# Kernel optimization log

Measured on AMD Instinct MI355X. Metric: run time of the kernel, lower is better.

The kernel has to match this reference:

```python
import jax, jax.numpy as jnp
import numpy as np

jax.config.update("jax_enable_x64", True)

B, H, W = 16384, 19, 19
MAX_FLOOD = min(H * W // 4, 100)  # = 90, as in the torch module


def _count_neighbors(m):
    # m: [B,H,W] float. Sum of 4 orthogonal neighbors (zero-padded edges).
    up = jnp.pad(m[:, :-1, :], ((0, 0), (1, 0), (0, 0)))
    down = jnp.pad(m[:, 1:, :], ((0, 0), (0, 1), (0, 0)))
    left = jnp.pad(m[:, :, :-1], ((0, 0), (0, 0), (1, 0)))
    right = jnp.pad(m[:, :, 1:], ((0, 0), (0, 0), (0, 1)))
    return up + down + left + right


def _dilate(m):
    # m: [B,H,W] bool. OR of 4 orthogonal neighbors (False-padded edges).
    up = jnp.pad(m[:, :-1, :], ((0, 0), (1, 0), (0, 0)))
    down = jnp.pad(m[:, 1:, :], ((0, 0), (0, 1), (0, 0)))
    left = jnp.pad(m[:, :, :-1], ((0, 0), (0, 0), (1, 0)))
    right = jnp.pad(m[:, :, 1:], ((0, 0), (0, 0), (0, 1)))
    return up | down | left | right


def _flood_fill(seeds, mask):
    # Iterative neighbor expansion within mask, bounded iters + early exit.
    def cond(st):
        _, changed, i = st
        return changed & (i < MAX_FLOOD)

    def body(st):
        g, _, i = st
        exp = _dilate(g) & mask & ~g
        return (g | exp, exp.any(), i + 1)

    g, _, _ = jax.lax.while_loop(cond, body, (seeds, seeds.any(), jnp.int32(0)))
    return g


def setup_inputs() -> dict:
    key = jax.random.key(0)
    k1, k2, k3, k4, k5, k6 = jax.random.split(key, 6)
    # 0 = empty, 1 = black, 2 = white (planes never overlap)
    board = jax.random.randint(k1, (B, H, W), 0, 3)
    stones = jnp.stack([board == 1, board == 2], axis=1).astype(jnp.float32)
    current_player = jax.random.randint(k2, (B,), 0, 2).astype(jnp.int32)
    ko_rc = jax.random.randint(k3, (B, 2), 0, H).astype(jnp.int32)
    has_ko = jax.random.uniform(k4, (B,)) < 0.25
    ko_points = jnp.where(has_ko[:, None], ko_rc, jnp.int32(-1))
    hmax = np.iinfo(np.int64).max
    zobrist_stones = jax.random.randint(k5, (2, H, W), 0, hmax, dtype=jnp.int64)
    zobrist_turn = jax.random.randint(k6, (2,), 0, hmax, dtype=jnp.int64)
    position_hash = jnp.zeros((B,), jnp.int64)
    return {
        "stones": stones,
        "current_player": current_player,
        "ko_points": ko_points,
        "zobrist_stones": zobrist_stones,
        "zobrist_turn": zobrist_turn,
        "position_hash": position_hash,
    }


def reference(stones, current_player, ko_points, zobrist_stones, zobrist_turn, position_hash):
    stones_b = stones > 0.5                       # [B,2,H,W] bool
    empty_f = 1.0 - stones.sum(axis=1)            # [B,H,W] float (0/1)
    empty = ~stones_b.any(axis=1)                 # empty_mask
    liberties = _count_neighbors(empty_f)         # float liberty count per point

    # legal = empty points with at least one empty neighbor
    legal = empty & (liberties > 0.0)

    # capture moves: opponent stones with exactly one liberty
    cp = current_player.astype(jnp.int32)
    opp = jnp.take_along_axis(stones_b, (1 - cp)[:, None, None, None], axis=1)[:, 0]
    vulnerable = opp & (jnp.round(liberties).astype(jnp.int32) == 1)
    cap = empty & (_count_neighbors(vulnerable.astype(jnp.float32)) > 0.0)
    legal = legal | cap

    # ko restriction: mask the single ko point per game (if set)
    valid_ko = ko_points[:, 0] >= 0
    r_eq = jnp.arange(H)[None, :, None] == ko_points[:, 0][:, None, None]
    c_eq = jnp.arange(W)[None, None, :] == ko_points[:, 1][:, None, None]
    legal = legal & ~(valid_ko[:, None, None] & r_eq & c_eq)

    # flood fill the full groups-in-atari within opponent stones
    groups = _flood_fill(vulnerable, opp)

    # zobrist hash: XOR of stone hashes over the board + turn toggle
    contrib = jnp.where(stones_b, zobrist_stones[None], jnp.int64(0))  # [B,2,H,W]
    board_hash = jax.lax.reduce(contrib, np.int64(0), jax.lax.bitwise_xor, (1, 2, 3))
    new_hash = position_hash ^ board_hash ^ zobrist_turn[cp] ^ zobrist_turn[1 - cp]

    return (liberties, legal, groups, new_hash)
```

## Files before the change

kernel.cpp:

```cpp
#include <hip/hip_runtime.h>
#include <stdint.h>

#define WW 19
#define NP 361
#define M19 0x7FFFFu
#define BPB 16
#define TPB 256
#define BBSTR 25
#define PLSTR 97

__device__ __forceinline__ uint32_t rev19(uint32_t x) { return __brev(x) >> 13; }

__device__ __forceinline__ uint32_t runfill(uint32_t g, uint32_t m) {
  const uint32_t up = g | (m & ((m + g) ^ m ^ g));
  const uint32_t rm = rev19(m);
  const uint32_t rg = rev19(g);
  const uint32_t dn = rg | (rm & ((rm + rg) ^ rm ^ rg));
  return up | rev19(dn);
}

__global__ __launch_bounds__(TPB, 2) void go_fused(
    const float* __restrict__ stones, const int* __restrict__ cur,
    const int* __restrict__ ko, const int* __restrict__ zob,
    const int* __restrict__ zturn, const int* __restrict__ phash,
    float* __restrict__ out, int B) {
  __shared__ uint32_t bbuf[BPB * BBSTR];
  __shared__ uint32_t pl[BPB * PLSTR];

  const int wid = threadIdx.x >> 6;
  const int lane = threadIdx.x & 63;
  const int b0 = blockIdx.x * BPB;
  const size_t NB = (size_t)B * NP;

  int zb[6], zw[6];
#pragma unroll
  for (int i = 0; i < 6; ++i) {
    const int p = i * 64 + lane;
    zb[i] = (p < NP) ? zob[p] : 0;
    zw[i] = (p < NP) ? zob[NP + p] : 0;
  }
  const int zt = zturn[0] ^ zturn[1];

  int acc[4];
#pragma unroll
  for (int k = 0; k < 4; ++k) {
    const int lb = wid * 4 + k;
    const int b = b0 + lb;
    acc[k] = 0;
    if (b < B) {
      const float* sb = stones + (size_t)b * (2 * NP);
#pragma unroll
      for (int i = 0; i < 6; ++i) {
        const int p = i * 64 + lane;
        const bool inb = p < NP;
        const float bv = inb ? sb[p] : 0.0f;
        const float wv = inb ? sb[NP + p] : 0.0f;
        const bool bs = bv > 0.5f, wsn = wv > 0.5f;
        const uint64_t bbm = __ballot(bs);
        const uint64_t wbm = __ballot(wsn);
        if (lane < 4) {
          const uint64_t src = (lane < 2) ? bbm : wbm;
          const uint32_t vv = (lane & 1) ? (uint32_t)(src >> 32) : (uint32_t)src;
          bbuf[lb * BBSTR + i * 4 + lane] = vv;
        }
        acc[k] ^= zb[i] & (bs ? -1 : 0);
        acc[k] ^= zw[i] & (wsn ? -1 : 0);
      }
    }
  }
#pragma unroll
  for (int off = 32; off > 0; off >>= 1) {
#pragma unroll
    for (int k = 0; k < 4; ++k) acc[k] ^= __shfl_xor(acc[k], off, 64);
  }
  if (lane == 0) {
#pragma unroll
    for (int k = 0; k < 4; ++k) {
      const int b = b0 + wid * 4 + k;
      if (b < B) out[3 * NB + b] = (float)(phash[b] ^ acc[k] ^ zt);
    }
  }
  __syncthreads();

  if (threadIdx.x < BPB) {
    const int lb = threadIdx.x;
    const int b = b0 + lb;
    if (b < B) {
      uint64_t bmw[6], wmw[6];
#pragma unroll
      for (int i = 0; i < 6; ++i) {
        const uint32_t* q = &bbuf[lb * BBSTR + 4 * i];
        bmw[i] = (uint64_t)q[0] | ((uint64_t)q[1] << 32);
        wmw[i] = (uint64_t)q[2] | ((uint64_t)q[3] << 32);
      }
      const int cp = cur[b];
      uint32_t m[WW], e[WW];
#pragma unroll
      for (int r = 0; r < WW; ++r) {
        const int bit = WW * r;
        const int w = bit >> 6, sh = bit & 63;
        uint64_t xb = bmw[w] >> sh;
        uint64_t xw = wmw[w] >> sh;
        if (sh > 45) { xb |= bmw[w + 1] << (64 - sh); xw |= wmw[w + 1] << (64 - sh); }
        const uint32_t br = (uint32_t)xb & M19;
        const uint32_t wr = (uint32_t)xw & M19;
        m[r] = (cp == 0) ? wr : br;
        e[r] = ~(br | wr) & M19;
      }

      uint32_t* pb = &pl[lb * PLSTR];
      uint32_t vul[WW];
#pragma unroll
      for (int r = 0; r < WW; ++r) {
        const uint32_t u = (r > 0) ? e[r - 1] : 0u;
        const uint32_t d = (r < WW - 1) ? e[r + 1] : 0u;
        const uint32_t l = (e[r] << 1) & M19;
        const uint32_t rr = e[r] >> 1;
        const uint32_t s1 = u ^ d, c1 = u & d;
        const uint32_t s2 = l ^ rr, c2 = l & rr;
        const uint32_t cc = s1 & s2;
        const uint32_t L0 = s1 ^ s2;
        const uint32_t L1 = c1 ^ c2 ^ cc;
        pb[r] = L0;
        pb[19 + r] = L1;
        pb[38 + r] = (c1 & c2) | (cc & (c1 | c2));
        vul[r] = m[r] & L0 & ~L1;
      }

      const int2 kk = ((const int2*)ko)[b];
#pragma unroll
      for (int r = 0; r < WW; ++r) {
        const uint32_t u = (r > 0) ? e[r - 1] : 0u;
        const uint32_t d = (r < WW - 1) ? e[r + 1] : 0u;
        const uint32_t nbv = ((r > 0) ? vul[r - 1] : 0u) |
                             ((r < WW - 1) ? vul[r + 1] : 0u) |
                             ((vul[r] << 1) & M19) | (vul[r] >> 1);
        uint32_t leg = e[r] & (u | d | ((e[r] << 1) & M19) | (e[r] >> 1));
        leg |= e[r] & nbv;
        if (kk.x == r) leg &= ~(1u << kk.y);
        pb[57 + r] = leg;
      }

      uint32_t g[WW];
#pragma unroll
      for (int r = 0; r < WW; ++r) g[r] = runfill(vul[r], m[r]);
      for (int it = 0; it < 45; ++it) {
        uint32_t chg = 0, prev = 0;
#pragma unroll
        for (int r = 0; r < WW; ++r) {
          uint32_t t = g[r] | (prev & m[r]);
          t = runfill(t, m[r]);
          chg |= t ^ g[r];
          g[r] = t;
          prev = t;
        }
        prev = 0;
#pragma unroll
        for (int r = WW - 1; r >= 0; --r) {
          uint32_t t = g[r] | (prev & m[r]);
          t = runfill(t, m[r]);
          chg |= t ^ g[r];
          g[r] = t;
          prev = t;
        }
        if (!__any(chg != 0u)) break;
      }
#pragma unroll
      for (int r = 0; r < WW; ++r) pb[76 + r] = g[r];
    }
  }
  __syncthreads();

  if (b0 + BPB <= B) {
    float4* s0 = (float4*)(out + (size_t)b0 * NP);
    float4* s1 = (float4*)(out + NB + (size_t)b0 * NP);
    float4* s2 = (float4*)(out + 2 * NB + (size_t)b0 * NP);
    const int nq = BPB * NP / 4;
    for (int q = threadIdx.x; q < nq; q += TPB) {
      float t0[4], t1[4], t2[4];
#pragma unroll
      for (int j = 0; j < 4; ++j) {
        const int id = q * 4 + j;
        const int lb = (id * 92949) >> 25;
        const int p = id - lb * NP;
        const int r = (p * 27) >> 9;
        const int c = p - r * WW;
        const uint32_t* pb = &pl[lb * PLSTR];
        const uint32_t l0 = (pb[r] >> c) & 1u;
        const uint32_t l1 = (pb[19 + r] >> c) & 1u;
        const uint32_t l2 = (pb[38 + r] >> c) & 1u;
        t0[j] = (float)(l0 + 2u * l1 + 4u * l2);
        t1[j] = (float)((pb[57 + r] >> c) & 1u);
        t2[j] = (float)((pb[76 + r] >> c) & 1u);
      }
      s0[q] = make_float4(t0[0], t0[1], t0[2], t0[3]);
      s1[q] = make_float4(t1[0], t1[1], t1[2], t1[3]);
      s2[q] = make_float4(t2[0], t2[1], t2[2], t2[3]);
    }
  } else {
#pragma unroll
    for (int k = 0; k < 4; ++k) {
      const int lb = wid * 4 + k;
      const int b = b0 + lb;
      if (b < B) {
        float* o0 = out + (size_t)b * NP;
        const uint32_t* pb = &pl[lb * PLSTR];
#pragma unroll
        for (int i = 0; i < 6; ++i) {
          const int p = i * 64 + lane;
          if (p < NP) {
            const int r = (p * 27) >> 9;
            const int c = p - r * WW;
            const uint32_t l0 = (pb[r] >> c) & 1u;
            const uint32_t l1 = (pb[19 + r] >> c) & 1u;
            const uint32_t l2 = (pb[38 + r] >> c) & 1u;
            o0[p] = (float)(l0 + 2u * l1 + 4u * l2);
            o0[NB + p] = (float)((pb[57 + r] >> c) & 1u);
            o0[2 * NB + p] = (float)((pb[76 + r] >> c) & 1u);
          }
        }
      }
    }
  }
}

extern "C" void kernel_launch(void* const* d_in, const int* in_sizes, int n_in,
                              void* d_out, int out_size, void* d_ws,
                              size_t ws_size, hipStream_t stream) {
  const float* stones = (const float*)d_in[0];
  const int* cur = (const int*)d_in[1];
  const int* ko = (const int*)d_in[2];
  const int* zob = (const int*)d_in[3];
  const int* zturn = (const int*)d_in[4];
  const int* phash = (const int*)d_in[5];
  float* out = (float*)d_out;

  const int B = in_sizes[0] / (2 * NP);
  const int blocks = (B + BPB - 1) / BPB;
  go_fused<<<blocks, TPB, 0, stream>>>(stones, cur, ko, zob, zturn, phash, out,
                                       B);
}
```

Measured before the change: 32.74 us.

## Parallelize per-board bitboard work across lanes, one lane per row

Previously only 16 threads per block ran the liberty, legality and flood-fill work, one thread per board looping over all 19 rows. Now each wave handles 3 boards with one lane per row (57 active lanes), exchanging neighbor rows through wave shuffles. The flood fill becomes a parallel row-step iteration with a wave-wide exit check, and occupancy bounds rise to 4. The trade-off is that the fill may need more iterations than the old up/down sweep, blocks shrink to 12 boards, and 7 lanes per wave sit idle.

Result: faster. 29.76 us (-9.1%).

```diff
diff --git a/kernel.cpp b/kernel.cpp
--- a/kernel.cpp
+++ b/kernel.cpp
@@ -4,7 +4,9 @@
 #define WW 19
 #define NP 361
 #define M19 0x7FFFFu
-#define BPB 16
+#define BPW 3
+#define NWAVES 4
+#define BPB (BPW * NWAVES)
 #define TPB 256
 #define BBSTR 25
 #define PLSTR 97
@@ -19,7 +21,7 @@
   return up | rev19(dn);
 }
 
-__global__ __launch_bounds__(TPB, 2) void go_fused(
+__global__ __launch_bounds__(TPB, 4) void go_fused(
     const float* __restrict__ stones, const int* __restrict__ cur,
     const int* __restrict__ ko, const int* __restrict__ zob,
     const int* __restrict__ zturn, const int* __restrict__ phash,
@@ -41,10 +43,10 @@
   }
   const int zt = zturn[0] ^ zturn[1];
 
-  int acc[4];
-#pragma unroll
-  for (int k = 0; k < 4; ++k) {
-    const int lb = wid * 4 + k;
+  int acc[BPW];
+#pragma unroll
+  for (int k = 0; k < BPW; ++k) {
+    const int lb = wid * BPW + k;
     const int b = b0 + lb;
     acc[k] = 0;
     if (b < B) {
@@ -71,102 +73,90 @@
 #pragma unroll
   for (int off = 32; off > 0; off >>= 1) {
 #pragma unroll
-    for (int k = 0; k < 4; ++k) acc[k] ^= __shfl_xor(acc[k], off, 64);
+    for (int k = 0; k < BPW; ++k) acc[k] ^= __shfl_xor(acc[k], off, 64);
   }
   if (lane == 0) {
 #pragma unroll
-    for (int k = 0; k < 4; ++k) {
-      const int b = b0 + wid * 4 + k;
+    for (int k = 0; k < BPW; ++k) {
+      const int b = b0 + wid * BPW + k;
       if (b < B) out[3 * NB + b] = (float)(phash[b] ^ acc[k] ^ zt);
     }
   }
   __syncthreads();
 
-  if (threadIdx.x < BPB) {
-    const int lb = threadIdx.x;
+  {
+    const int k = (lane * 27) >> 9;
+    const int r = lane - k * WW;
+    const int lb = wid * BPW + k;
     const int b = b0 + lb;
-    if (b < B) {
-      uint64_t bmw[6], wmw[6];
-#pragma unroll
-      for (int i = 0; i < 6; ++i) {
-        const uint32_t* q = &bbuf[lb * BBSTR + 4 * i];
-        bmw[i] = (uint64_t)q[0] | ((uint64_t)q[1] << 32);
-        wmw[i] = (uint64_t)q[2] | ((uint64_t)q[3] << 32);
-      }
-      const int cp = cur[b];
-      uint32_t m[WW], e[WW];
-#pragma unroll
-      for (int r = 0; r < WW; ++r) {
-        const int bit = WW * r;
-        const int w = bit >> 6, sh = bit & 63;
-        uint64_t xb = bmw[w] >> sh;
-        uint64_t xw = wmw[w] >> sh;
-        if (sh > 45) { xb |= bmw[w + 1] << (64 - sh); xw |= wmw[w + 1] << (64 - sh); }
-        const uint32_t br = (uint32_t)xb & M19;
-        const uint32_t wr = (uint32_t)xw & M19;
-        m[r] = (cp == 0) ? wr : br;
-        e[r] = ~(br | wr) & M19;
-      }
-
+    const bool vl = (lane < 57) && (b < B);
+    const int lbs = vl ? lb : 0;
+    const int bsafe = vl ? b : (B - 1);
+
+    const int cp = cur[bsafe];
+    const int2 kk = ((const int2*)ko)[bsafe];
+
+    uint32_t mrow, erow;
+    {
+      const int bit = WW * r;
+      const int w = bit >> 6, sh = bit & 63;
+      const uint32_t* q = &bbuf[lbs * BBSTR + 4 * w];
+      const uint64_t Blo = (uint64_t)q[0] | ((uint64_t)q[1] << 32);
+      const uint64_t Wlo = (uint64_t)q[2] | ((uint64_t)q[3] << 32);
+      uint32_t br = (uint32_t)(Blo >> sh);
+      uint32_t wr = (uint32_t)(Wlo >> sh);
+      if (sh > 45) {
+        const uint64_t Bhi = (uint64_t)q[4] | ((uint64_t)q[5] << 32);
+        const uint64_t Whi = (uint64_t)q[6] | ((uint64_t)q[7] << 32);
+        br |= (uint32_t)(Bhi << (64 - sh));
+        wr |= (uint32_t)(Whi << (64 - sh));
+      }
+      br &= M19;
+      wr &= M19;
+      mrow = vl ? ((cp == 0) ? wr : br) : 0u;
+      erow = vl ? (~(br | wr) & M19) : 0u;
+    }
+
+    uint32_t t;
+    t = __shfl(erow, lane - 1, 64);
+    const uint32_t eu = (r > 0) ? t : 0u;
+    t = __shfl(erow, lane + 1, 64);
+    const uint32_t ed = (r < 18) ? t : 0u;
+    const uint32_t el = (erow << 1) & M19;
+    const uint32_t er_ = erow >> 1;
+    const uint32_t s1 = eu ^ ed, c1 = eu & ed;
+    const uint32_t s2 = el ^ er_, c2 = el & er_;
+    const uint32_t cc = s1 & s2;
+    const uint32_t L0 = s1 ^ s2;
+    const uint32_t L1 = c1 ^ c2 ^ cc;
+    const uint32_t L2 = (c1 & c2) | (cc & (c1 | c2));
+    uint32_t leg = erow & (eu | ed | el | er_);
+    const uint32_t vul = mrow & L0 & ~L1;
+    t = __shfl(vul, lane - 1, 64);
+    const uint32_t vu = (r > 0) ? t : 0u;
+    t = __shfl(vul, lane + 1, 64);
+    const uint32_t vd = (r < 18) ? t : 0u;
+    leg |= erow & (vu | vd | ((vul << 1) & M19) | (vul >> 1));
+    if (kk.x == r) leg &= ~(1u << kk.y);
+
+    uint32_t g = runfill(vul, mrow);
+    for (int it = 0; it < 90; ++it) {
+      t = __shfl(g, lane - 1, 64);
+      const uint32_t gu = (r > 0) ? t : 0u;
+      t = __shfl(g, lane + 1, 64);
+      const uint32_t gd = (r < 18) ? t : 0u;
+      const uint32_t gn = runfill(g | ((gu | gd) & mrow), mrow);
+      if (!__any(gn != g)) break;
+      g = gn;
+    }
+
+    if (vl) {
       uint32_t* pb = &pl[lb * PLSTR];
-      uint32_t vul[WW];
-#pragma unroll
-      for (int r = 0; r < WW; ++r) {
-        const uint32_t u = (r > 0) ? e[r - 1] : 0u;
-        const uint32_t d = (r < WW - 1) ? e[r + 1] : 0u;
-        const uint32_t l = (e[r] << 1) & M19;
-        const uint32_t rr = e[r] >> 1;
-        const uint32_t s1 = u ^ d, c1 = u & d;
-        const uint32_t s2 = l ^ rr, c2 = l & rr;
-        const uint32_t cc = s1 & s2;
-        const uint32_t L0 = s1 ^ s2;
-        const uint32_t L1 = c1 ^ c2 ^ cc;
-        pb[r] = L0;
-        pb[19 + r] = L1;
-        pb[38 + r] = (c1 & c2) | (cc & (c1 | c2));
-        vul[r] = m[r] & L0 & ~L1;
-      }
-
-      const int2 kk = ((const int2*)ko)[b];
-#pragma unroll
-      for (int r = 0; r < WW; ++r) {
-        const uint32_t u = (r > 0) ? e[r - 1] : 0u;
-        const uint32_t d = (r < WW - 1) ? e[r + 1] : 0u;
-        const uint32_t nbv = ((r > 0) ? vul[r - 1] : 0u) |
-                             ((r < WW - 1) ? vul[r + 1] : 0u) |
-                             ((vul[r] << 1) & M19) | (vul[r] >> 1);
-        uint32_t leg = e[r] & (u | d | ((e[r] << 1) & M19) | (e[r] >> 1));
-        leg |= e[r] & nbv;
-        if (kk.x == r) leg &= ~(1u << kk.y);
-        pb[57 + r] = leg;
-      }
-
-      uint32_t g[WW];
-#pragma unroll
-      for (int r = 0; r < WW; ++r) g[r] = runfill(vul[r], m[r]);
-      for (int it = 0; it < 45; ++it) {
-        uint32_t chg = 0, prev = 0;
-#pragma unroll
-        for (int r = 0; r < WW; ++r) {
-          uint32_t t = g[r] | (prev & m[r]);
-          t = runfill(t, m[r]);
-          chg |= t ^ g[r];
-          g[r] = t;
-          prev = t;
-        }
-        prev = 0;
-#pragma unroll
-        for (int r = WW - 1; r >= 0; --r) {
-          uint32_t t = g[r] | (prev & m[r]);
-          t = runfill(t, m[r]);
-          chg |= t ^ g[r];
-          g[r] = t;
-          prev = t;
-        }
-        if (!__any(chg != 0u)) break;
-      }
-#pragma unroll
-      for (int r = 0; r < WW; ++r) pb[76 + r] = g[r];
+      pb[r] = L0;
+      pb[19 + r] = L1;
+      pb[38 + r] = L2;
+      pb[57 + r] = leg;
+      pb[76 + r] = g;
     }
   }
   __syncthreads();
@@ -199,8 +189,8 @@
     }
   } else {
 #pragma unroll
-    for (int k = 0; k < 4; ++k) {
-      const int lb = wid * 4 + k;
+    for (int k = 0; k < BPW; ++k) {
+      const int lb = wid * BPW + k;
       const int b = b0 + lb;
       if (b < B) {
         float* o0 = out + (size_t)b * NP;
```
